# Kernel tuning notes

Measured on AMD Instinct MI355X. Metric: run time of the kernel, lower is better.

Reference implementation:

```python
import jax, jax.numpy as jnp
import numpy as np

EPS = 1e-5      # batch-norm epsilon
ALPHA = 0.2     # leaky_relu negative slope


def bn_lrelu(h, gamma, beta):
    # training-mode batch norm over the batch axis, then leaky relu
    mean = jnp.mean(h, axis=0)
    var = jnp.var(h, axis=0)
    h = (h - mean) * jax.lax.rsqrt(var + EPS) * gamma + beta
    return jnp.where(h >= 0, h, ALPHA * h)


def setup_inputs() -> dict:
    key = jax.random.key(0)
    ks = jax.random.split(key, 16)
    O, T, Din, H, Dout = 50000, 200000, 128, 512, 128
    s = 0.02
    inp = {
        "obj_vecs": jax.random.normal(ks[0], (O, Din), jnp.float32),
        "pred_vecs": jax.random.normal(ks[1], (T, Din), jnp.float32),
        "edges": jax.random.randint(ks[2], (T, 2), 0, O, jnp.int64),
        # net1: [3*Din -> H -> 2H+Dout], each Linear followed by BN + leaky_relu
        "W1a": jax.random.normal(ks[3], (3 * Din, H), jnp.float32) * s,
        "b1a": jnp.zeros((H,), jnp.float32),
        "g1a": jnp.ones((H,), jnp.float32),
        "be1a": jnp.zeros((H,), jnp.float32),
        "W1b": jax.random.normal(ks[4], (H, 2 * H + Dout), jnp.float32) * s,
        "b1b": jnp.zeros((2 * H + Dout,), jnp.float32),
        "g1b": jnp.ones((2 * H + Dout,), jnp.float32),
        "be1b": jnp.zeros((2 * H + Dout,), jnp.float32),
        # net2: [H -> H -> Dout]
        "W2a": jax.random.normal(ks[5], (H, H), jnp.float32) * s,
        "b2a": jnp.zeros((H,), jnp.float32),
        "g2a": jnp.ones((H,), jnp.float32),
        "be2a": jnp.zeros((H,), jnp.float32),
        "W2b": jax.random.normal(ks[6], (H, Dout), jnp.float32) * s,
        "b2b": jnp.zeros((Dout,), jnp.float32),
        "g2b": jnp.ones((Dout,), jnp.float32),
        "be2b": jnp.zeros((Dout,), jnp.float32),
    }
    return inp


def reference(obj_vecs, pred_vecs, edges,
              W1a, b1a, g1a, be1a, W1b, b1b, g1b, be1b,
              W2a, b2a, g2a, be2a, W2b, b2b, g2b, be2b):
    O = obj_vecs.shape[0]
    H = W1a.shape[1]
    Dout = W2b.shape[1]
    s_idx = edges[:, 0]
    o_idx = edges[:, 1]

    # gather subject/object vecs and concat with predicate vecs: [T, 3*Din]
    cur_t = jnp.concatenate([obj_vecs[s_idx], pred_vecs, obj_vecs[o_idx]], axis=1)

    # net1 MLP
    h = bn_lrelu(cur_t @ W1a + b1a, g1a, be1a)           # [T, H]
    new_t = bn_lrelu(h @ W1b + b1b, g1b, be1b)            # [T, 2H+Dout]

    new_s = new_t[:, :H]
    new_p = new_t[:, H:H + Dout]
    new_o = new_t[:, H + Dout:]

    # scatter-add pooling back to objects, then average
    pooled = jnp.zeros((O, H), jnp.float32).at[s_idx].add(new_s).at[o_idx].add(new_o)
    counts = jnp.zeros((O,), jnp.float32).at[s_idx].add(1.0).at[o_idx].add(1.0)
    counts = jnp.clip(counts, 1.0, float(O))
    pooled = pooled / counts[:, None]

    # net2 MLP
    h2 = bn_lrelu(pooled @ W2a + b2a, g2a, be2a)          # [O, H]
    new_obj = bn_lrelu(h2 @ W2b + b2b, g2b, be2b)         # [O, Dout]
    return new_obj, new_p
```

## Files before the change

kernel.cpp:

```cpp
#include <hip/hip_runtime.h>

typedef __bf16 bf16;
typedef __bf16 bf16x4 __attribute__((ext_vector_type(4)));
typedef __bf16 bf16x8 __attribute__((ext_vector_type(8)));
typedef float  f32x4  __attribute__((ext_vector_type(4)));

#define BM 128
#define BN 128
#define BKT 64
#define LDT 72

#ifndef __has_builtin
#define __has_builtin(x) 0
#endif

#if __has_builtin(__builtin_amdgcn_global_load_lds)
#define GLL16(srcp, basep) \
  __builtin_amdgcn_global_load_lds( \
      (const __attribute__((address_space(1))) unsigned int*)(srcp), \
      (__attribute__((address_space(3))) unsigned int*)(basep), 16, 0, 0)
#else
#define GLL16(srcp, basep) \
  (((bf16x8*)(basep))[lane] = *(const bf16x8*)(srcp))
#endif

template<int AMODE, int EPI>
__global__ __launch_bounds__(256) void gemm_k(
    const bf16* __restrict__ Abf, const float* __restrict__ Af32,
    const float* __restrict__ obj, const float* __restrict__ pred,
    const int* __restrict__ edges, const float* __restrict__ invcnt,
    const float* __restrict__ scale, const float* __restrict__ shift,
    const float* __restrict__ oscale, const float* __restrict__ oshift,
    const bf16* __restrict__ WT,
    bf16* __restrict__ outB, float* __restrict__ outF,
    float* __restrict__ pooled, float* __restrict__ gsum, float* __restrict__ gsq,
    int M, int N, int K, int rbase)
{
  __shared__ __align__(16) bf16 As[BM * 64];
  __shared__ __align__(16) bf16 Bs[BN * 64];
  __shared__ float sc_sh[(AMODE == 1) ? 512 : 1];
  __shared__ float sh_sh[(AMODE == 1) ? 512 : 1];
  __shared__ float osc[(EPI == 2 || EPI == 5) ? BN : 1];
  __shared__ float osh[(EPI == 2 || EPI == 5) ? BN : 1];
  __shared__ int eS[(AMODE == 0 || EPI == 2) ? BM : 1];
  __shared__ int eO[(AMODE == 0 || EPI == 2) ? BM : 1];

  const int tid = threadIdx.x;

  int bx = blockIdx.x, by = blockIdx.y;
  {
    const int NX = gridDim.x, NY = gridDim.y;
    int L = by * NX + bx;
    int bpg = NX * 8;
    int nFull = NY >> 3;
    int Lfull = nFull * bpg;
    if (L < Lfull) {
      int g = L / bpg, w2 = L - g * bpg;
      by = (g << 3) + (w2 & 7);
      bx = w2 >> 3;
    } else {
      int r2 = L - Lfull;
      int q = r2 / NX;
      by = (nFull << 3) + q;
      bx = r2 - q * NX;
    }
  }
  const int m0 = rbase + by * BM;
  const int n0 = bx * BN;

  const int lane = tid & 63;
  const int w = tid >> 6;
  const int wm = (w >> 1) * 64;
  const int wn = (w & 1) * 64;
  const int l15 = lane & 15;
  const int quad = lane >> 4;

  if (AMODE == 1) {
    for (int c = tid; c < K; c += 256) { sc_sh[c] = scale[c]; sh_sh[c] = shift[c]; }
  }
  if (EPI == 2 || EPI == 5) {
    if (tid < BN) { osc[tid] = oscale[n0 + tid]; osh[tid] = oshift[n0 + tid]; }
  }
  if (AMODE == 0 || EPI == 2) {
    if (tid < BM) {
      int r = m0 + tid; if (r >= M) r = M - 1;
      eS[tid] = edges[2 * r];
      eO[tid] = edges[2 * r + 1];
    }
  }
  __syncthreads();

  f32x4 acc[4][4];
  #pragma unroll
  for (int i = 0; i < 4; ++i)
    #pragma unroll
    for (int j = 0; j < 4; ++j)
      acc[i][j] = (f32x4){0.f, 0.f, 0.f, 0.f};

  const int rsub = lane >> 3;
  const int cch  = lane & 7;

  for (int k0 = 0; k0 < K; k0 += BKT) {
    #pragma unroll
    for (int it = 0; it < 4; ++it) {
      int blk = it * 4 + w;
      int r = blk * 8 + rsub;
      int cs = cch ^ (r & 7);
      const bf16* src = WT + (size_t)(n0 + r) * K + k0 + cs * 8;
      GLL16(src, &Bs[blk * 512]);
    }
    if (AMODE == 3) {
      #pragma unroll
      for (int it = 0; it < 4; ++it) {
        int blk = it * 4 + w;
        int r = blk * 8 + rsub;
        int row = m0 + r; if (row >= M) row = M - 1;
        int cs = cch ^ (r & 7);
        const bf16* src = Abf + (size_t)row * K + k0 + cs * 8;
        GLL16(src, &As[blk * 512]);
      }
    } else if (AMODE == 1) {
      int idx = tid;
      #pragma unroll
      for (int it = 0; it < 4; ++it, idx += 256) {
        int r = idx >> 3, ch = idx & 7;
        int row = m0 + r; if (row >= M) row = M - 1;
        bf16x8 v = *reinterpret_cast<const bf16x8*>(Abf + (size_t)row * K + k0 + ch * 8);
        bf16x8 o;
        #pragma unroll
        for (int e = 0; e < 8; ++e) {
          int c = k0 + ch * 8 + e;
          float f = sc_sh[c] * (float)v[e] + sh_sh[c];
          f = f >= 0.f ? f : 0.2f * f;
          o[e] = (bf16)f;
        }
        *reinterpret_cast<bf16x8*>(&As[r * 64 + ((ch ^ (r & 7)) << 3)]) = o;
      }
    } else {
      int idx = tid;
      #pragma unroll
      for (int it = 0; it < 8; ++it, idx += 256) {
        int r = idx >> 4, c4 = (idx & 15) << 2;
        int row = m0 + r; if (row >= M) row = M - 1;
        const float* src;
        float mul = 1.f;
        if (AMODE == 0) {
          int k = k0 + c4;
          if (k < 128)      src = obj  + (size_t)eS[r] * 128 + k;
          else if (k < 256) src = pred + (size_t)row * 128 + (k - 128);
          else              src = obj  + (size_t)eO[r] * 128 + (k - 256);
        } else {
          src = Af32 + (size_t)row * K + k0 + c4;
          mul = invcnt[row];
        }
        float4 v = *reinterpret_cast<const float4*>(src);
        bf16x4 o;
        o[0] = (bf16)(v.x * mul); o[1] = (bf16)(v.y * mul);
        o[2] = (bf16)(v.z * mul); o[3] = (bf16)(v.w * mul);
        int ch = c4 >> 3;
        int half = (c4 >> 2) & 1;
        *reinterpret_cast<bf16x4*>(&As[r * 64 + ((ch ^ (r & 7)) << 3) + (half << 2)]) = o;
      }
    }
    __syncthreads();
    #pragma unroll
    for (int kk = 0; kk < BKT; kk += 32) {
      bf16x8 af[4], bfv[4];
      #pragma unroll
      for (int i = 0; i < 4; ++i) {
        int r = wm + i * 16 + l15;
        int ci = (kk >> 3) + quad;
        af[i] = *reinterpret_cast<const bf16x8*>(&As[r * 64 + ((ci ^ (r & 7)) << 3)]);
      }
      #pragma unroll
      for (int j = 0; j < 4; ++j) {
        int r = wn + j * 16 + l15;
        int ci = (kk >> 3) + quad;
        bfv[j] = *reinterpret_cast<const bf16x8*>(&Bs[r * 64 + ((ci ^ (r & 7)) << 3)]);
      }
      #pragma unroll
      for (int i = 0; i < 4; ++i)
        #pragma unroll
        for (int j = 0; j < 4; ++j)
          acc[i][j] = __builtin_amdgcn_mfma_f32_16x16x32_bf16(af[i], bfv[j], acc[i][j], 0, 0, 0);
    }
    __syncthreads();
  }

  if (EPI == 2) {
    #pragma unroll
    for (int i = 0; i < 4; ++i) {
      #pragma unroll
      for (int r = 0; r < 4; ++r) {
        int lrow = wm + i * 16 + quad * 4 + r;
        int row = m0 + lrow;
        if (row >= M) continue;
        #pragma unroll
        for (int j = 0; j < 4; ++j) {
          int cl = wn + j * 16 + l15;
          int n1 = n0 + cl;
          float v = osc[cl] * acc[i][j][r] + osh[cl];
          v = v >= 0.f ? v : 0.2f * v;
          if (n1 < 512)      atomicAdd(&pooled[(size_t)eS[lrow] * 512 + n1], v);
          else if (n1 < 640) outF[(size_t)row * 128 + (n1 - 512)] = v;
          else               atomicAdd(&pooled[(size_t)eO[lrow] * 512 + (n1 - 640)], v);
        }
      }
    }
  } else if (EPI == 5) {
    #pragma unroll
    for (int i = 0; i < 4; ++i) {
      #pragma unroll
      for (int r = 0; r < 4; ++r) {
        int lrow = wm + i * 16 + quad * 4 + r;
        int row = m0 + lrow;
        if (row >= M) continue;
        #pragma unroll
        for (int j = 0; j < 4; ++j) {
          int cl = wn + j * 16 + l15;
          int n1 = n0 + cl;
          float v = osc[cl] * acc[i][j][r] + osh[cl];
          v = v >= 0.f ? v : 0.2f * v;
          if (n1 < 512)      outB[(size_t)(row - rbase) * 1024 + n1] = (bf16)v;
          else if (n1 < 640) outF[(size_t)row * 128 + (n1 - 512)] = v;
          else               outB[(size_t)(row - rbase) * 1024 + (n1 - 128)] = (bf16)v;
        }
      }
    }
  } else {
    #pragma unroll
    for (int j = 0; j < 4; ++j) {
      float s = 0.f, q = 0.f;
      #pragma unroll
      for (int i = 0; i < 4; ++i) {
        #pragma unroll
        for (int r = 0; r < 4; ++r) {
          int row = m0 + wm + i * 16 + quad * 4 + r;
          if (row >= M) continue;
          float v = acc[i][j][r];
          s += v; q += v * v;
          int col = n0 + wn + j * 16 + l15;
          if (EPI == 0) outB[(size_t)row * N + col] = (bf16)v;
          if (EPI == 3) outF[(size_t)row * N + col] = v;
        }
      }
      s += __shfl_xor(s, 16); q += __shfl_xor(q, 16);
      s += __shfl_xor(s, 32); q += __shfl_xor(q, 32);
      if (quad == 0) {
        int col = n0 + wn + j * 16 + l15;
        atomicAdd(&gsum[col], s);
        atomicAdd(&gsq[col], q);
      }
    }
  }
}

__global__ __launch_bounds__(256) void gatherc_k(const bf16* __restrict__ buf,
    const int* __restrict__ rowptr, const int* __restrict__ list,
    float* __restrict__ pooled, int c0, int c1, int O) {
  int o = blockIdx.x * 4 + (threadIdx.x >> 6);
  if (o >= O) return;
  int lane = threadIdx.x & 63;
  int cc = lane * 8;
  int e0 = rowptr[o], e1 = rowptr[o + 1];
  float acc[8];
  #pragma unroll
  for (int j = 0; j < 8; ++j) acc[j] = 0.f;
  bool any = false;
  for (int e = e0; e < e1; ++e) {
    int id = list[e];
    int t = id >> 1;
    if (t < c0 || t >= c1) continue;
    const bf16* row = buf + (size_t)(t - c0) * 1024 + (id & 1) * 512 + cc;
    bf16x8 v = *reinterpret_cast<const bf16x8*>(row);
    #pragma unroll
    for (int j = 0; j < 8; ++j) acc[j] += (float)v[j];
    any = true;
  }
  if (!any) return;
  float* dst = pooled + (size_t)o * 512 + cc;
  float4 a = *reinterpret_cast<float4*>(dst);
  float4 b = *reinterpret_cast<float4*>(dst + 4);
  a.x += acc[0]; a.y += acc[1]; a.z += acc[2]; a.w += acc[3];
  b.x += acc[4]; b.y += acc[5]; b.z += acc[6]; b.w += acc[7];
  *reinterpret_cast<float4*>(dst) = a;
  *reinterpret_cast<float4*>(dst + 4) = b;
}

__global__ __launch_bounds__(256) void gram_k(const bf16* __restrict__ A2,
                                              float* __restrict__ G, int T) {
  __shared__ __align__(16) bf16 Ks[2][128][LDT];
  const int tid = threadIdx.x;
  const int tile = blockIdx.x % 10;
  const int s    = blockIdx.x / 10;
  const int NS   = gridDim.x / 10;
  const int K1T[10] = {0, 0, 0, 0, 1, 1, 1, 2, 2, 3};
  const int K2T[10] = {0, 1, 2, 3, 1, 2, 3, 2, 3, 3};
  const int k1b = K1T[tile], k2b = K2T[tile];
  const int lane = tid & 63;
  const int w = tid >> 6;
  const int wm = (w >> 1) * 64;
  const int wn = (w & 1) * 64;
  const int l15 = lane & 15;
  const int quad = lane >> 4;

  const int NG = (T + 63) >> 6;
  const int GPB = (NG + NS - 1) / NS;
  const int g0 = s * GPB;
  const int gend = min(NG, g0 + GPB);

  f32x4 acc[4][4];
  #pragma unroll
  for (int i = 0; i < 4; ++i)
    #pragma unroll
    for (int j = 0; j < 4; ++j)
      acc[i][j] = (f32x4){0.f, 0.f, 0.f, 0.f};

  const int bsel = (k1b == k2b) ? 0 : 1;

  for (int g = g0; g < gend; ++g) {
    const int t0 = g << 6;
    #pragma unroll
    for (int it = 0; it < 4; ++it) {
      int lin = it * 256 + tid;
      int t = lin >> 4, c8 = lin & 15;
      int row = t0 + t;
      bf16x8 v;
      #pragma unroll
      for (int e = 0; e < 8; ++e) v[e] = (bf16)0.f;
      if (row < T)
        v = *reinterpret_cast<const bf16x8*>(A2 + (size_t)row * 512 + k1b * 128 + c8 * 8);
      int ts = t ^ ((c8 & 7) << 3);
      #pragma unroll
      for (int e = 0; e < 8; ++e) Ks[0][c8 * 8 + e][ts] = v[e];
    }
    if (bsel) {
      #pragma unroll
      for (int it = 0; it < 4; ++it) {
        int lin = it * 256 + tid;
        int t = lin >> 4, c8 = lin & 15;
        int row = t0 + t;
        bf16x8 v;
        #pragma unroll
        for (int e = 0; e < 8; ++e) v[e] = (bf16)0.f;
        if (row < T)
          v = *reinterpret_cast<const bf16x8*>(A2 + (size_t)row * 512 + k2b * 128 + c8 * 8);
        int ts = t ^ ((c8 & 7) << 3);
        #pragma unroll
        for (int e = 0; e < 8; ++e) Ks[1][c8 * 8 + e][ts] = v[e];
      }
    }
    __syncthreads();
    #pragma unroll
    for (int kk = 0; kk < 64; kk += 32) {
      bf16x8 af[4], bfv[4];
      #pragma unroll
      for (int i = 0; i < 4; ++i) {
        int r = wm + i * 16 + l15;
        int toff = (kk + quad * 8) ^ (((r >> 3) & 7) << 3);
        af[i] = *reinterpret_cast<const bf16x8*>(&Ks[0][r][toff]);
      }
      #pragma unroll
      for (int j = 0; j < 4; ++j) {
        int r = wn + j * 16 + l15;
        int toff = (kk + quad * 8) ^ (((r >> 3) & 7) << 3);
        bfv[j] = *reinterpret_cast<const bf16x8*>(&Ks[bsel][r][toff]);
      }
      #pragma unroll
      for (int i = 0; i < 4; ++i)
        #pragma unroll
        for (int j = 0; j < 4; ++j)
          acc[i][j] = __builtin_amdgcn_mfma_f32_16x16x32_bf16(af[i], bfv[j], acc[i][j], 0, 0, 0);
    }
    __syncthreads();
  }

  #pragma unroll
  for (int i = 0; i < 4; ++i) {
    #pragma unroll
    for (int r = 0; r < 4; ++r) {
      int grow = k1b * 128 + wm + i * 16 + quad * 4 + r;
      #pragma unroll
      for (int j = 0; j < 4; ++j) {
        int gcol = k2b * 128 + wn + j * 16 + l15;
        float v = acc[i][j][r];
        atomicAdd(&G[(size_t)grow * 512 + gcol], v);
        if (k1b != k2b)
          atomicAdd(&G[(size_t)gcol * 512 + grow], v);
      }
    }
  }
}

__global__ __launch_bounds__(256) void act_colsum_k(bf16* __restrict__ hA,
    const float* __restrict__ scale, const float* __restrict__ shift,
    float* __restrict__ csum, int T) {
  __shared__ float sh[4 * 512];
  const int tid = threadIdx.x;
  const int c0 = (tid & 63) * 8;
  const int rofs = tid >> 6;
  float sc[8], sf[8];
  #pragma unroll
  for (int j = 0; j < 8; ++j) { sc[j] = scale[c0 + j]; sf[j] = shift[c0 + j]; }
  float acc[8];
  #pragma unroll
  for (int j = 0; j < 8; ++j) acc[j] = 0.f;
  for (int r = blockIdx.x * 4 + rofs; r < T; r += gridDim.x * 4) {
    bf16x8 v = *reinterpret_cast<const bf16x8*>(hA + (size_t)r * 512 + c0);
    bf16x8 o;
    #pragma unroll
    for (int j = 0; j < 8; ++j) {
      float f = sc[j] * (float)v[j] + sf[j];
      f = f >= 0.f ? f : 0.2f * f;
      o[j] = (bf16)f;
      acc[j] += (float)o[j];
    }
    *reinterpret_cast<bf16x8*>(hA + (size_t)r * 512 + c0) = o;
  }
  #pragma unroll
  for (int j = 0; j < 8; ++j) sh[rofs * 512 + c0 + j] = acc[j];
  __syncthreads();
  for (int c = tid; c < 512; c += 256) {
    float s = sh[c] + sh[512 + c] + sh[1024 + c] + sh[1536 + c];
    atomicAdd(&csum[c], s);
  }
}

__global__ __launch_bounds__(256) void colstat_k(const float* __restrict__ G,
    const float* __restrict__ csum, const float* __restrict__ W1b,
    float* __restrict__ sumB, float* __restrict__ sqB) {
  __shared__ float wL[4][512];
  __shared__ float rq[4][4], rs[4][4];
  const int tid = threadIdx.x;
  const int c0 = blockIdx.x * 4;
  for (int idx = tid; idx < 2048; idx += 256) {
    int c = idx >> 9, k = idx & 511;
    wL[c][k] = W1b[(size_t)k * 1152 + c0 + c];
  }
  __syncthreads();
  float pq[4] = {0.f, 0.f, 0.f, 0.f};
  float ps[4] = {0.f, 0.f, 0.f, 0.f};
  for (int e = tid; e < 512 * 512; e += 256) {
    int i = e >> 9, j = e & 511;
    float g = G[e];
    #pragma unroll
    for (int c = 0; c < 4; ++c) pq[c] += g * wL[c][i] * wL[c][j];
  }
  for (int k = tid; k < 512; k += 256) {
    float cs = csum[k];
    #pragma unroll
    for (int c = 0; c < 4; ++c) ps[c] += cs * wL[c][k];
  }
  #pragma unroll
  for (int c = 0; c < 4; ++c) {
    #pragma unroll
    for (int off = 32; off > 0; off >>= 1) {
      pq[c] += __shfl_xor(pq[c], off);
      ps[c] += __shfl_xor(ps[c], off);
    }
  }
  const int w = tid >> 6, lane = tid & 63;
  if (lane == 0) {
    #pragma unroll
    for (int c = 0; c < 4; ++c) { rq[w][c] = pq[c]; rs[w][c] = ps[c]; }
  }
  __syncthreads();
  if (tid < 4) {
    sqB[c0 + tid]  = rq[0][tid] + rq[1][tid] + rq[2][tid] + rq[3][tid];
    sumB[c0 + tid] = rs[0][tid] + rs[1][tid] + rs[2][tid] + rs[3][tid];
  }
}

__global__ __launch_bounds__(256) void tconv_k(const float* __restrict__ W,
                                               bf16* __restrict__ WT, int K, int N) {
  int idx = blockIdx.x * 256 + threadIdx.x;
  if (idx < K * N) {
    int n = idx / K, k = idx - n * K;
    WT[(size_t)n * K + k] = (bf16)W[(size_t)k * N + n];
  }
}

__global__ __launch_bounds__(256) void bnfin_k(const float* __restrict__ sum,
    const float* __restrict__ sq, const float* __restrict__ g,
    const float* __restrict__ be, float* __restrict__ scale,
    float* __restrict__ shift, int C, float invR) {
  int c = blockIdx.x * 256 + threadIdx.x;
  if (c < C) {
    float m = sum[c] * invR;
    float v = sq[c] * invR - m * m;
    float a = g[c] * rsqrtf(v + 1e-5f);
    scale[c] = a;
    shift[c] = be[c] - m * a;
  }
}

__global__ __launch_bounds__(256) void cntint_k(const int* __restrict__ edges,
                                                int* __restrict__ cnt, int T) {
  int t = blockIdx.x * 256 + threadIdx.x;
  if (t < T) {
    atomicAdd(&cnt[edges[2 * t]], 1);
    atomicAdd(&cnt[edges[2 * t + 1]], 1);
  }
}

__global__ __launch_bounds__(256) void invcnt_k(const int* __restrict__ cnt,
                                                float* __restrict__ invc, int O) {
  int i = blockIdx.x * 256 + threadIdx.x;
  if (i < O) {
    float c = fminf(fmaxf((float)cnt[i], 1.f), (float)O);
    invc[i] = 1.f / c;
  }
}

__global__ __launch_bounds__(1024) void scan_k(const int* __restrict__ cnt,
    int* __restrict__ rowptr, int* __restrict__ head, int O, int total) {
  __shared__ int sh[1024];
  const int t = threadIdx.x;
  const int C = (O + 1023) / 1024;
  const int i0 = t * C;
  int s = 0;
  for (int i = 0; i < C; ++i) { int idx = i0 + i; if (idx < O) s += cnt[idx]; }
  sh[t] = s;
  __syncthreads();
  for (int d = 1; d < 1024; d <<= 1) {
    int v = (t >= d) ? sh[t - d] : 0;
    __syncthreads();
    sh[t] += v;
    __syncthreads();
  }
  int run = (t == 0) ? 0 : sh[t - 1];
  for (int i = 0; i < C; ++i) {
    int idx = i0 + i;
    if (idx < O) { rowptr[idx] = run; head[idx] = run; run += cnt[idx]; }
  }
  if (t == 0) rowptr[O] = total;
}

__global__ __launch_bounds__(256) void fill_k(const int* __restrict__ edges,
    int* __restrict__ head, int* __restrict__ list, int T) {
  int t = blockIdx.x * 256 + threadIdx.x;
  if (t < T) {
    int s = edges[2 * t];
    int p = atomicAdd(&head[s], 1);
    list[p] = t << 1;
    int o = edges[2 * t + 1];
    p = atomicAdd(&head[o], 1);
    list[p] = (t << 1) | 1;
  }
}

__global__ __launch_bounds__(256) void final_k(float* __restrict__ buf,
    const float* __restrict__ scale, const float* __restrict__ shift, int n) {
  int i = blockIdx.x * 256 + threadIdx.x;
  if (i < n) {
    int c = i & 127;
    float v = scale[c] * buf[i] + shift[c];
    buf[i] = v >= 0.f ? v : 0.2f * v;
  }
}

extern "C" void kernel_launch(void* const* d_in, const int* in_sizes, int n_in,
                              void* d_out, int out_size, void* d_ws, size_t ws_size,
                              hipStream_t stream) {
  const float* obj   = (const float*)d_in[0];
  const float* pred  = (const float*)d_in[1];
  const int*   edges = (const int*)d_in[2];
  const float* W1a = (const float*)d_in[3];
  const float* g1a = (const float*)d_in[5];
  const float* be1a= (const float*)d_in[6];
  const float* W1b = (const float*)d_in[7];
  const float* g1b = (const float*)d_in[9];
  const float* be1b= (const float*)d_in[10];
  const float* W2a = (const float*)d_in[11];
  const float* g2a = (const float*)d_in[13];
  const float* be2a= (const float*)d_in[14];
  const float* W2b = (const float*)d_in[15];
  const float* g2b = (const float*)d_in[17];
  const float* be2b= (const float*)d_in[18];

  const int O = in_sizes[0] / 128;
  const int T = in_sizes[1] / 128;
  float* out_obj = (float*)d_out;
  float* out_p   = (float*)d_out + (size_t)O * 128;

  char* base = (char*)d_ws;
  size_t off = 0;
  auto alloc = [&](size_t bytes) { size_t p = off; off += (bytes + 255) & ~(size_t)255; return p; };
  size_t oWT1a = alloc((size_t)384 * 512 * 2);
  size_t oWT1b = alloc((size_t)512 * 1152 * 2);
  size_t oWT2a = alloc((size_t)512 * 512 * 2);
  size_t oWT2b = alloc((size_t)512 * 128 * 2);
  size_t oSums = alloc(4608 * 4);
  size_t oScl  = alloc(4608 * 4);
  size_t oG    = alloc((size_t)512 * 512 * 4);
  size_t oCsum = alloc(512 * 4);
  size_t oCnt  = alloc((size_t)O * 4);
  size_t oInvc = alloc((size_t)O * 4);
  size_t oRp   = alloc((size_t)(O + 1) * 4);
  size_t oHead = alloc((size_t)O * 4);
  size_t oList = alloc((size_t)2 * T * 4);
  size_t oHA   = alloc((size_t)T * 512 * 2);
  size_t oPool = off;
  size_t oBuf  = oPool + (((size_t)O * 512 * 4 + 255) & ~(size_t)255);

  int chunkT = 0;
  if (ws_size > oBuf) {
    size_t ct = (ws_size - oBuf) / 2048;
    if (ct > (size_t)T) ct = T;
    chunkT = (int)(ct & ~(size_t)127);
  }
  const bool chunked = (chunkT >= 8192);

  bf16* WT1a = (bf16*)(base + oWT1a);
  bf16* WT1b = (bf16*)(base + oWT1b);
  bf16* WT2a = (bf16*)(base + oWT2a);
  bf16* WT2b = (bf16*)(base + oWT2b);
  float* sums = (float*)(base + oSums);
  float* sumA = sums,        * sqA = sums + 512;
  float* sumB = sums + 1024, * sqB = sums + 2176;
  float* sumC = sums + 3328, * sqC = sums + 3840;
  float* sumD = sums + 4352, * sqD = sums + 4480;
  float* scl = (float*)(base + oScl);
  float* scaleA = scl,        * shiftA = scl + 512;
  float* scaleB = scl + 1024, * shiftB = scl + 2176;
  float* scaleC = scl + 3328, * shiftC = scl + 3840;
  float* scaleD = scl + 4352, * shiftD = scl + 4480;
  float* Gm   = (float*)(base + oG);
  float* csum = (float*)(base + oCsum);
  int*   cntI = (int*)(base + oCnt);
  float* invc = (float*)(base + oInvc);
  int*   rowptr = (int*)(base + oRp);
  int*   head = (int*)(base + oHead);
  int*   list = (int*)(base + oList);
  bf16*  hA = (bf16*)(base + oHA);
  bf16*  h2 = (bf16*)(base + oHA);
  float* pooledF = (float*)(base + oPool);
  bf16*  buf = (bf16*)(base + oBuf);
  float* objpre = out_obj;

  hipMemsetAsync(sums, 0, 4608 * 4, stream);
  hipMemsetAsync(cntI, 0, (size_t)O * 4, stream);
  hipMemsetAsync(Gm, 0, (size_t)512 * 512 * 4, stream);
  hipMemsetAsync(csum, 0, 512 * 4, stream);
  hipMemsetAsync(pooledF, 0, (size_t)O * 512 * 4, stream);

  tconv_k<<<(384 * 512 + 255) / 256, 256, 0, stream>>>(W1a, WT1a, 384, 512);
  tconv_k<<<(512 * 1152 + 255) / 256, 256, 0, stream>>>(W1b, WT1b, 512, 1152);
  tconv_k<<<(512 * 512 + 255) / 256, 256, 0, stream>>>(W2a, WT2a, 512, 512);
  tconv_k<<<(512 * 128 + 255) / 256, 256, 0, stream>>>(W2b, WT2b, 512, 128);
  cntint_k<<<(T + 255) / 256, 256, 0, stream>>>(edges, cntI, T);
  invcnt_k<<<(O + 255) / 256, 256, 0, stream>>>(cntI, invc, O);
  if (chunked) {
    scan_k<<<1, 1024, 0, stream>>>(cntI, rowptr, head, O, 2 * T);
    fill_k<<<(T + 255) / 256, 256, 0, stream>>>(edges, head, list, T);
  }

  const int Tb = (T + BM - 1) / BM;
  const int Ob = (O + BM - 1) / BM;

  {
    dim3 g(512 / BN, Tb);
    gemm_k<0, 0><<<g, 256, 0, stream>>>(nullptr, nullptr, obj, pred, edges, nullptr,
        nullptr, nullptr, nullptr, nullptr, WT1a, hA, nullptr, nullptr, sumA, sqA,
        T, 512, 384, 0);
  }
  bnfin_k<<<2, 256, 0, stream>>>(sumA, sqA, g1a, be1a, scaleA, shiftA, 512, 1.f / T);

  act_colsum_k<<<1024, 256, 0, stream>>>(hA, scaleA, shiftA, csum, T);
  gram_k<<<10 * 48, 256, 0, stream>>>(hA, Gm, T);
  colstat_k<<<288, 256, 0, stream>>>(Gm, csum, W1b, sumB, sqB);
  bnfin_k<<<5, 256, 0, stream>>>(sumB, sqB, g1b, be1b, scaleB, shiftB, 1152, 1.f / T);

  if (chunked) {
    for (int c0 = 0; c0 < T; c0 += chunkT) {
      int c1 = min(T, c0 + chunkT);
      dim3 g(1152 / BN, (c1 - c0 + BM - 1) / BM);
      gemm_k<3, 5><<<g, 256, 0, stream>>>(hA, nullptr, nullptr, nullptr, nullptr,
          nullptr, nullptr, nullptr, scaleB, shiftB, WT1b, buf, out_p, nullptr,
          nullptr, nullptr, c1, 1152, 512, c0);
      gatherc_k<<<(O + 3) / 4, 256, 0, stream>>>(buf, rowptr, list, pooledF, c0, c1, O);
    }
  } else {
    dim3 g(1152 / BN, Tb);
    gemm_k<3, 2><<<g, 256, 0, stream>>>(hA, nullptr, nullptr, nullptr, edges, nullptr,
        nullptr, nullptr, scaleB, shiftB, WT1b, nullptr, out_p, pooledF, nullptr,
        nullptr, T, 1152, 512, 0);
  }

  {
    dim3 g(512 / BN, Ob);
    gemm_k<2, 0><<<g, 256, 0, stream>>>(nullptr, pooledF, nullptr, nullptr, nullptr,
        invc, nullptr, nullptr, nullptr, nullptr, WT2a, h2, nullptr, nullptr,
        sumC, sqC, O, 512, 512, 0);
  }
  bnfin_k<<<2, 256, 0, stream>>>(sumC, sqC, g2a, be2a, scaleC, shiftC, 512, 1.f / O);

  {
    dim3 g(128 / BN, Ob);
    gemm_k<1, 3><<<g, 256, 0, stream>>>(h2, nullptr, nullptr, nullptr, nullptr, nullptr,
        scaleC, shiftC, nullptr, nullptr, WT2b, nullptr, objpre, nullptr, sumD, sqD,
        O, 128, 512, 0);
  }
  bnfin_k<<<1, 256, 0, stream>>>(sumD, sqD, g2b, be2b, scaleD, shiftD, 128, 1.f / O);

  final_k<<<((size_t)O * 128 + 255) / 256, 256, 0, stream>>>(objpre, scaleD, shiftD,
      (int)((size_t)O * 128));
}
```

Measured before the change: 2.028 ms.

## Pre-convert inputs to bf16, transpose activations for Gram GEMM, bf16 pooled input

Converts obj and pred vectors to bf16 up front so the first GEMM can gather rows with async global-to-LDS loads. In the chunked path, the BN-activation pass now also writes a transposed chunk, so a new Gram kernel can load contiguous tiles with global_load_lds instead of scattering into LDS. The pooled sums are converted to bf16, already scaled by inverse counts, so the net2 GEMM uses the fast bf16 A path. These steps add extra conversion kernels and reuse workspace buffers (A2T aliases pooledF, so the memset is moved later), which adds aliasing risk.

Result: slower. 2.222 ms (+9.6%).

```diff
diff --git a/kernel.cpp b/kernel.cpp
--- a/kernel.cpp
+++ b/kernel.cpp
@@ -42,8 +42,8 @@
   __shared__ float sh_sh[(AMODE == 1) ? 512 : 1];
   __shared__ float osc[(EPI == 2 || EPI == 5) ? BN : 1];
   __shared__ float osh[(EPI == 2 || EPI == 5) ? BN : 1];
-  __shared__ int eS[(AMODE == 0 || EPI == 2) ? BM : 1];
-  __shared__ int eO[(AMODE == 0 || EPI == 2) ? BM : 1];
+  __shared__ int eS[(AMODE == 0 || AMODE == 5 || EPI == 2) ? BM : 1];
+  __shared__ int eO[(AMODE == 0 || AMODE == 5 || EPI == 2) ? BM : 1];
 
   const int tid = threadIdx.x;
 
@@ -81,7 +81,7 @@
   if (EPI == 2 || EPI == 5) {
     if (tid < BN) { osc[tid] = oscale[n0 + tid]; osh[tid] = oshift[n0 + tid]; }
   }
-  if (AMODE == 0 || EPI == 2) {
+  if (AMODE == 0 || AMODE == 5 || EPI == 2) {
     if (tid < BM) {
       int r = m0 + tid; if (r >= M) r = M - 1;
       eS[tid] = edges[2 * r];
@@ -117,6 +117,22 @@
         int row = m0 + r; if (row >= M) row = M - 1;
         int cs = cch ^ (r & 7);
         const bf16* src = Abf + (size_t)row * K + k0 + cs * 8;
+        GLL16(src, &As[blk * 512]);
+      }
+    } else if (AMODE == 5) {
+      const bf16* objB  = (const bf16*)obj;
+      const bf16* predB = (const bf16*)pred;
+      #pragma unroll
+      for (int it = 0; it < 4; ++it) {
+        int blk = it * 4 + w;
+        int r = blk * 8 + rsub;
+        int row = m0 + r; if (row >= M) row = M - 1;
+        int cs = cch ^ (r & 7);
+        int k = k0 + cs * 8;
+        const bf16* src;
+        if (k0 < 128)      src = objB  + (size_t)eS[r] * 128 + k;
+        else if (k0 < 256) src = predB + (size_t)row * 128 + (k - 128);
+        else               src = objB  + (size_t)eO[r] * 128 + (k - 256);
         GLL16(src, &As[blk * 512]);
       }
     } else if (AMODE == 1) {
@@ -255,6 +271,195 @@
   }
 }
 
+__global__ __launch_bounds__(256) void convf2b_k(const float* __restrict__ src,
+    bf16* __restrict__ dst, size_t n8) {
+  size_t i = (size_t)blockIdx.x * 256 + threadIdx.x;
+  if (i < n8) {
+    const float4* s = reinterpret_cast<const float4*>(src + i * 8);
+    float4 a = s[0], b = s[1];
+    bf16x8 o;
+    o[0] = (bf16)a.x; o[1] = (bf16)a.y; o[2] = (bf16)a.z; o[3] = (bf16)a.w;
+    o[4] = (bf16)b.x; o[5] = (bf16)b.y; o[6] = (bf16)b.z; o[7] = (bf16)b.w;
+    reinterpret_cast<bf16x8*>(dst)[i] = o;
+  }
+}
+
+__global__ __launch_bounds__(256) void pconv_k(const float* __restrict__ pooledF,
+    const float* __restrict__ invc, bf16* __restrict__ pooledB, int O) {
+  size_t i = (size_t)blockIdx.x * 256 + threadIdx.x;
+  if (i < (size_t)O * 64) {
+    int o = (int)(i >> 6);
+    float ic = invc[o];
+    const float4* s = reinterpret_cast<const float4*>(pooledF + i * 8);
+    float4 a = s[0], b = s[1];
+    bf16x8 v;
+    v[0] = (bf16)(a.x * ic); v[1] = (bf16)(a.y * ic);
+    v[2] = (bf16)(a.z * ic); v[3] = (bf16)(a.w * ic);
+    v[4] = (bf16)(b.x * ic); v[5] = (bf16)(b.y * ic);
+    v[6] = (bf16)(b.z * ic); v[7] = (bf16)(b.w * ic);
+    reinterpret_cast<bf16x8*>(pooledB)[i] = v;
+  }
+}
+
+__global__ __launch_bounds__(256) void trans_act_k(bf16* __restrict__ hA,
+    const float* __restrict__ scale, const float* __restrict__ shift,
+    float* __restrict__ csum, bf16* __restrict__ A2T,
+    int t0, int TCp, int T) {
+  __shared__ __align__(16) bf16 ld[32][520];
+  __shared__ float cs_sh[4][512];
+  const int tid = threadIdx.x;
+  const int c8 = (tid & 63) * 8;
+  const int rq = tid >> 6;
+  const int bt0 = t0 + blockIdx.x * 64;
+  const int tl = bt0 - t0;
+
+  float sc[8], sf[8];
+  #pragma unroll
+  for (int j = 0; j < 8; ++j) { sc[j] = scale[c8 + j]; sf[j] = shift[c8 + j]; }
+  float acc[8];
+  #pragma unroll
+  for (int j = 0; j < 8; ++j) acc[j] = 0.f;
+
+  #pragma unroll
+  for (int sub = 0; sub < 2; ++sub) {
+    #pragma unroll
+    for (int i = 0; i < 8; ++i) {
+      int r = rq * 8 + i;
+      int row = bt0 + sub * 32 + r;
+      bf16x8 o;
+      if (row < T) {
+        bf16x8 v = *reinterpret_cast<const bf16x8*>(hA + (size_t)row * 512 + c8);
+        #pragma unroll
+        for (int j = 0; j < 8; ++j) {
+          float f = sc[j] * (float)v[j] + sf[j];
+          f = f >= 0.f ? f : 0.2f * f;
+          o[j] = (bf16)f;
+          acc[j] += (float)o[j];
+        }
+        *reinterpret_cast<bf16x8*>(hA + (size_t)row * 512 + c8) = o;
+      } else {
+        #pragma unroll
+        for (int j = 0; j < 8; ++j) o[j] = (bf16)0.f;
+      }
+      *reinterpret_cast<bf16x8*>(&ld[r][c8]) = o;
+    }
+    __syncthreads();
+    for (int cc = tid; cc < 512; cc += 256) {
+      #pragma unroll
+      for (int g8 = 0; g8 < 4; ++g8) {
+        bf16x8 o;
+        #pragma unroll
+        for (int e = 0; e < 8; ++e) o[e] = ld[g8 * 8 + e][cc];
+        *reinterpret_cast<bf16x8*>(A2T + (size_t)cc * TCp + tl + sub * 32 + g8 * 8) = o;
+      }
+    }
+    __syncthreads();
+  }
+  #pragma unroll
+  for (int j = 0; j < 8; ++j) cs_sh[rq][c8 + j] = acc[j];
+  __syncthreads();
+  for (int c = tid; c < 512; c += 256) {
+    float s = cs_sh[0][c] + cs_sh[1][c] + cs_sh[2][c] + cs_sh[3][c];
+    atomicAdd(&csum[c], s);
+  }
+}
+
+__global__ __launch_bounds__(256) void gram2_k(const bf16* __restrict__ A2T,
+    float* __restrict__ G, int TCp, int NS) {
+  __shared__ __align__(16) bf16 As[128 * 64];
+  __shared__ __align__(16) bf16 Bs[128 * 64];
+  const int tid = threadIdx.x;
+  const int pair = blockIdx.x % 10;
+  const int s    = blockIdx.x / 10;
+  const int K1T[10] = {0, 0, 0, 0, 1, 1, 1, 2, 2, 3};
+  const int K2T[10] = {0, 1, 2, 3, 1, 2, 3, 2, 3, 3};
+  const int k1b = K1T[pair], k2b = K2T[pair];
+  const int lane = tid & 63;
+  const int w = tid >> 6;
+  const int wm = (w >> 1) * 64;
+  const int wn = (w & 1) * 64;
+  const int l15 = lane & 15;
+  const int quad = lane >> 4;
+  const int rsub = lane >> 3;
+  const int cch  = lane & 7;
+
+  const int NG = TCp >> 6;
+  const int GPB = (NG + NS - 1) / NS;
+  const int g0 = s * GPB;
+  const int gend = min(NG, g0 + GPB);
+  if (g0 >= gend) return;
+
+  f32x4 acc[4][4];
+  #pragma unroll
+  for (int i = 0; i < 4; ++i)
+    #pragma unroll
+    for (int j = 0; j < 4; ++j)
+      acc[i][j] = (f32x4){0.f, 0.f, 0.f, 0.f};
+
+  const bool diag = (k1b == k2b);
+  const bf16* BsP = diag ? As : Bs;
+
+  for (int g = g0; g < gend; ++g) {
+    const int t0 = g << 6;
+    #pragma unroll
+    for (int it = 0; it < 4; ++it) {
+      int blk = it * 4 + w;
+      int r = blk * 8 + rsub;
+      int cs = cch ^ (r & 7);
+      const bf16* src = A2T + (size_t)(k1b * 128 + r) * TCp + t0 + cs * 8;
+      GLL16(src, &As[blk * 512]);
+    }
+    if (!diag) {
+      #pragma unroll
+      for (int it = 0; it < 4; ++it) {
+        int blk = it * 4 + w;
+        int r = blk * 8 + rsub;
+        int cs = cch ^ (r & 7);
+        const bf16* src = A2T + (size_t)(k2b * 128 + r) * TCp + t0 + cs * 8;
+        GLL16(src, &Bs[blk * 512]);
+      }
+    }
+    __syncthreads();
+    #pragma unroll
+    for (int kk = 0; kk < 64; kk += 32) {
+      bf16x8 af[4], bfv[4];
+      #pragma unroll
+      for (int i = 0; i < 4; ++i) {
+        int r = wm + i * 16 + l15;
+        int ci = (kk >> 3) + quad;
+        af[i] = *reinterpret_cast<const bf16x8*>(&As[r * 64 + ((ci ^ (r & 7)) << 3)]);
+      }
+      #pragma unroll
+      for (int j = 0; j < 4; ++j) {
+        int r = wn + j * 16 + l15;
+        int ci = (kk >> 3) + quad;
+        bfv[j] = *reinterpret_cast<const bf16x8*>(&BsP[r * 64 + ((ci ^ (r & 7)) << 3)]);
+      }
+      #pragma unroll
+      for (int i = 0; i < 4; ++i)
+        #pragma unroll
+        for (int j = 0; j < 4; ++j)
+          acc[i][j] = __builtin_amdgcn_mfma_f32_16x16x32_bf16(af[i], bfv[j], acc[i][j], 0, 0, 0);
+    }
+    __syncthreads();
+  }
+
+  #pragma unroll
+  for (int i = 0; i < 4; ++i) {
+    #pragma unroll
+    for (int r = 0; r < 4; ++r) {
+      int grow = k1b * 128 + wm + i * 16 + quad * 4 + r;
+      #pragma unroll
+      for (int j = 0; j < 4; ++j) {
+        int gcol = k2b * 128 + wn + j * 16 + l15;
+        float v = acc[i][j][r];
+        atomicAdd(&G[(size_t)grow * 512 + gcol], v);
+        if (!diag) atomicAdd(&G[(size_t)gcol * 512 + grow], v);
+      }
+    }
+  }
+}
+
 __global__ __launch_bounds__(256) void gatherc_k(const bf16* __restrict__ buf,
     const int* __restrict__ rowptr, const int* __restrict__ list,
     float* __restrict__ pooled, int c0, int c1, int O) {
@@ -303,21 +508,17 @@
   const int wn = (w & 1) * 64;
   const int l15 = lane & 15;
   const int quad = lane >> 4;
-
   const int NG = (T + 63) >> 6;
   const int GPB = (NG + NS - 1) / NS;
   const int g0 = s * GPB;
   const int gend = min(NG, g0 + GPB);
-
   f32x4 acc[4][4];
   #pragma unroll
   for (int i = 0; i < 4; ++i)
     #pragma unroll
     for (int j = 0; j < 4; ++j)
       acc[i][j] = (f32x4){0.f, 0.f, 0.f, 0.f};
-
   const int bsel = (k1b == k2b) ? 0 : 1;
-
   for (int g = g0; g < gend; ++g) {
     const int t0 = g << 6;
     #pragma unroll
@@ -374,7 +575,6 @@
     }
     __syncthreads();
   }
-
   #pragma unroll
   for (int i = 0; i < 4; ++i) {
     #pragma unroll
@@ -610,6 +810,14 @@
     chunkT = (int)(ct & ~(size_t)127);
   }
   const bool chunked = (chunkT >= 8192);
+
+  long long crll = ((long long)O * 2 & ~63LL) - 64;
+  int chunkR = (int)(crll < 64 ? 64 : crll);
+  if (chunkR > T) chunkR = (T + 63) & ~63;
+
+  size_t objB_sz  = (((size_t)O * 128 * 2) + 255) & ~(size_t)255;
+  size_t predB_sz = (size_t)T * 128 * 2;
+  const bool canConv = chunked && (ws_size >= oBuf + objB_sz + predB_sz);
 
   bf16* WT1a = (bf16*)(base + oWT1a);
   bf16* WT1b = (bf16*)(base + oWT1b);
@@ -634,15 +842,19 @@
   int*   list = (int*)(base + oList);
   bf16*  hA = (bf16*)(base + oHA);
   bf16*  h2 = (bf16*)(base + oHA);
+  bf16*  pooledB = (bf16*)(base + oHA + (size_t)O * 512 * 4);
   float* pooledF = (float*)(base + oPool);
+  bf16*  A2T = (bf16*)(base + oPool);
   bf16*  buf = (bf16*)(base + oBuf);
+  bf16*  objB  = (bf16*)(base + oBuf);
+  bf16*  predB = (bf16*)(base + oBuf + objB_sz);
   float* objpre = out_obj;
 
   hipMemsetAsync(sums, 0, 4608 * 4, stream);
   hipMemsetAsync(cntI, 0, (size_t)O * 4, stream);
   hipMemsetAsync(Gm, 0, (size_t)512 * 512 * 4, stream);
   hipMemsetAsync(csum, 0, 512 * 4, stream);
-  hipMemsetAsync(pooledF, 0, (size_t)O * 512 * 4, stream);
+  if (!chunked) hipMemsetAsync(pooledF, 0, (size_t)O * 512 * 4, stream);
 
   tconv_k<<<(384 * 512 + 255) / 256, 256, 0, stream>>>(W1a, WT1a, 384, 512);
   tconv_k<<<(512 * 1152 + 255) / 256, 256, 0, stream>>>(W1b, WT1b, 512, 1152);
@@ -654,24 +866,39 @@
     scan_k<<<1, 1024, 0, stream>>>(cntI, rowptr, head, O, 2 * T);
     fill_k<<<(T + 255) / 256, 256, 0, stream>>>(edges, head, list, T);
   }
+  if (canConv) {
+    convf2b_k<<<(int)(((size_t)O * 16 + 255) / 256), 256, 0, stream>>>(obj, objB, (size_t)O * 16);
+    convf2b_k<<<(int)(((size_t)T * 16 + 255) / 256), 256, 0, stream>>>(pred, predB, (size_t)T * 16);
+  }
 
   const int Tb = (T + BM - 1) / BM;
   const int Ob = (O + BM - 1) / BM;
 
   {
     dim3 g(512 / BN, Tb);
-    gemm_k<0, 0><<<g, 256, 0, stream>>>(nullptr, nullptr, obj, pred, edges, nullptr,
-        nullptr, nullptr, nullptr, nullptr, WT1a, hA, nullptr, nullptr, sumA, sqA,
-        T, 512, 384, 0);
+    if (canConv)
+      gemm_k<5, 0><<<g, 256, 0, stream>>>(nullptr, nullptr, (const float*)objB,
+          (const float*)predB, edges, nullptr, nullptr, nullptr, nullptr, nullptr,
+          WT1a, hA, nullptr, nullptr, sumA, sqA, T, 512, 384, 0);
+    else
+      gemm_k<0, 0><<<g, 256, 0, stream>>>(nullptr, nullptr, obj, pred, edges, nullptr,
+          nullptr, nullptr, nullptr, nullptr, WT1a, hA, nullptr, nullptr, sumA, sqA,
+          T, 512, 384, 0);
   }
   bnfin_k<<<2, 256, 0, stream>>>(sumA, sqA, g1a, be1a, scaleA, shiftA, 512, 1.f / T);
 
-  act_colsum_k<<<1024, 256, 0, stream>>>(hA, scaleA, shiftA, csum, T);
-  gram_k<<<10 * 48, 256, 0, stream>>>(hA, Gm, T);
-  colstat_k<<<288, 256, 0, stream>>>(Gm, csum, W1b, sumB, sqB);
-  bnfin_k<<<5, 256, 0, stream>>>(sumB, sqB, g1b, be1b, scaleB, shiftB, 1152, 1.f / T);
-
   if (chunked) {
+    for (int t0 = 0; t0 < T; t0 += chunkR) {
+      int TC = min(T - t0, chunkR);
+      int TCp = (TC + 63) & ~63;
+      trans_act_k<<<TCp / 64, 256, 0, stream>>>(hA, scaleA, shiftA, csum, A2T,
+          t0, TCp, T);
+      gram2_k<<<10 * 64, 256, 0, stream>>>(A2T, Gm, TCp, 64);
+    }
+    colstat_k<<<288, 256, 0, stream>>>(Gm, csum, W1b, sumB, sqB);
+    bnfin_k<<<5, 256, 0, stream>>>(sumB, sqB, g1b, be1b, scaleB, shiftB, 1152, 1.f / T);
+
+    hipMemsetAsync(pooledF, 0, (size_t)O * 512 * 4, stream);
     for (int c0 = 0; c0 < T; c0 += chunkT) {
       int c1 = min(T, c0 + chunkT);
       dim3 g(1152 / BN, (c1 - c0 + BM - 1) / BM);
@@ -680,16 +907,25 @@
           nullptr, nullptr, c1, 1152, 512, c0);
       gatherc_k<<<(O + 3) / 4, 256, 0, stream>>>(buf, rowptr, list, pooledF, c0, c1, O);
     }
+    pconv_k<<<(int)(((size_t)O * 64 + 255) / 256), 256, 0, stream>>>(pooledF, invc,
+        pooledB, O);
+    {
+      dim3 g(512 / BN, Ob);
+      gemm_k<3, 0><<<g, 256, 0, stream>>>(pooledB, nullptr, nullptr, nullptr, nullptr,
+          nullptr, nullptr, nullptr, nullptr, nullptr, WT2a, h2, nullptr, nullptr,
+          sumC, sqC, O, 512, 512, 0);
+    }
   } else {
-    dim3 g(1152 / BN, Tb);
-    gemm_k<3, 2><<<g, 256, 0, stream>>>(hA, nullptr, nullptr, nullptr, edges, nullptr,
+    act_colsum_k<<<1024, 256, 0, stream>>>(hA, scaleA, shiftA, csum, T);
+    gram_k<<<10 * 48, 256, 0, stream>>>(hA, Gm, T);
+    colstat_k<<<288, 256, 0, stream>>>(Gm, csum, W1b, sumB, sqB);
+    bnfin_k<<<5, 256, 0, stream>>>(sumB, sqB, g1b, be1b, scaleB, shiftB, 1152, 1.f / T);
+    dim3 g2(1152 / BN, Tb);
+    gemm_k<3, 2><<<g2, 256, 0, stream>>>(hA, nullptr, nullptr, nullptr, edges, nullptr,
         nullptr, nullptr, scaleB, shiftB, WT1b, nullptr, out_p, pooledF, nullptr,
         nullptr, T, 1152, 512, 0);
-  }
-
-  {
-    dim3 g(512 / BN, Ob);
-    gemm_k<2, 0><<<g, 256, 0, stream>>>(nullptr, pooledF, nullptr, nullptr, nullptr,
+    dim3 g3(512 / BN, Ob);
+    gemm_k<2, 0><<<g3, 256, 0, stream>>>(nullptr, pooledF, nullptr, nullptr, nullptr,
         invc, nullptr, nullptr, nullptr, nullptr, WT2a, h2, nullptr, nullptr,
         sumC, sqC, O, 512, 512, 0);
   }
```
